# Optimization experiments

Hardware: AMD Instinct MI355X
Metric: run time of the kernel (lower is better)

The kernel has to match this reference:

```python
import jax, jax.numpy as jnp
import numpy as np
import math

HEAD_DIM = 128
NUM_Q_HEAD = 32
NUM_KV_HEAD = 8
WINDOW = 512
CAP = 30.0
CLIP_LO, CLIP_HI = -0.03, 1.03
EPS = 1e-5
SCALE = 1.0 / math.sqrt(HEAD_DIM)
B, S = 2, 2048


def group_rms_norm(x, w, group_size, eps):
    # x: [B, S, hidden]; normalize each contiguous group of size group_size
    Bx, Sx, H = x.shape
    ng = H // group_size
    xg = x.reshape(Bx, Sx, ng, group_size)
    inv = jax.lax.rsqrt(jnp.mean(xg * xg, axis=-1, keepdims=True) + eps)
    return (xg * inv).reshape(Bx, Sx, H) * w


def setup_inputs() -> dict:
    key = jax.random.key(0)
    kq, kk, kv, kw1, kw2 = jax.random.split(key, 5)
    q = jax.random.normal(kq, (B, S, NUM_Q_HEAD, HEAD_DIM), dtype=jnp.float32)
    k = jax.random.normal(kk, (B, S, NUM_KV_HEAD, HEAD_DIM), dtype=jnp.float32)
    v = jax.random.normal(kv, (B, S, NUM_KV_HEAD, HEAD_DIM), dtype=jnp.float32)
    # GroupRMSNorm weights, init uniform in (-1, 1)
    q_norm_w = jax.random.uniform(kw1, (NUM_Q_HEAD * HEAD_DIM,), dtype=jnp.float32, minval=-1.0, maxval=1.0)
    kv_norm_w = jax.random.uniform(kw2, (NUM_KV_HEAD * HEAD_DIM,), dtype=jnp.float32, minval=-1.0, maxval=1.0)
    return {"q": q, "k": k, "v": v, "q_norm_w": q_norm_w, "kv_norm_w": kv_norm_w}


def reference(q, k, v, q_norm_w, kv_norm_w):
    Bq, Sq, Hq, D = q.shape
    Sk = k.shape[1]
    # QK GroupRMSNorm over flattened hidden dim, group_size = head_dim
    qn = group_rms_norm(q.reshape(Bq, Sq, Hq * D), q_norm_w, HEAD_DIM, EPS).reshape(q.shape)
    kn = group_rms_norm(k.reshape(Bq, Sk, NUM_KV_HEAD * D), kv_norm_w, HEAD_DIM, EPS).reshape(k.shape)
    # GQA: repeat_interleave kv heads along head axis
    rep = Hq // NUM_KV_HEAD
    kr = jnp.repeat(kn, rep, axis=2)  # [B, Sk, Hq, D]
    vr = jnp.repeat(v, rep, axis=2)
    # scores: [B, Hq, Sq, Sk]
    scores = jnp.einsum("bqhd,bkhd->bhqk", qn, kr) * SCALE
    scores = CAP * jnp.tanh(scores / CAP)  # softmax capping
    # sliding-window + causal mask: allowed iff i - WINDOW <= j <= i (offset = Sk - Sq = 0)
    offset = Sk - Sq
    i = jnp.arange(Sq)[:, None] + offset
    j = jnp.arange(Sk)[None, :]
    allowed = (j <= i) & (j >= i - WINDOW)
    scores = jnp.where(allowed, scores, -jnp.inf)
    probs = jax.nn.softmax(scores, axis=-1)
    probs = jnp.nan_to_num(probs, nan=0.0)
    # softmax clipping
    probs = jnp.clip((CLIP_HI - CLIP_LO) * probs + CLIP_LO, 0.0, 1.0)
    out = jnp.einsum("bhqk,bkhd->bqhd", probs, vr)
    return out
```

## Files before the change

### kernel.cpp

```cpp
#include <hip/hip_runtime.h>

#define SEQ 2048
#define DD 128
#define HQ 32
#define HKV 8
#define WIN 512

typedef unsigned short u16;
typedef unsigned int u32;
typedef unsigned long long u64;
typedef __attribute__((ext_vector_type(8))) short bf16x8;
typedef __attribute__((ext_vector_type(4))) float f32x4;
typedef __attribute__((ext_vector_type(2))) float f32x2;

#define SBAR() asm volatile("s_barrier" ::: "memory")
#define WAITV0() asm volatile("s_waitcnt vmcnt(0)" ::: "memory")
#define WAITV4() asm volatile("s_waitcnt vmcnt(4)" ::: "memory")
#define WAITLGKM0() asm volatile("s_waitcnt lgkmcnt(0)" ::: "memory")

__device__ __forceinline__ u16 f2bf(float f) {
  u32 u = __builtin_bit_cast(u32, f);
  u += 0x7FFFu + ((u >> 16) & 1u);
  return (u16)(u >> 16);
}

__device__ __forceinline__ void gl16(const void* g, void* l) {
  __builtin_amdgcn_global_load_lds(
      (const __attribute__((address_space(1))) void*)g,
      (__attribute__((address_space(3))) void*)l, 16, 0, 0);
}

__device__ __forceinline__ u32 cvtpk(float lo, float hi) {
  u32 r;
  asm("v_cvt_pk_bf16_f32 %0, %1, %2" : "=v"(r) : "v"(lo), "v"(hi));
  return r;
}

__device__ __forceinline__ f32x2 pk_mul(f32x2 a, f32x2 b) {
  f32x2 d;
  asm("v_pk_mul_f32 %0, %1, %2" : "=v"(d) : "v"(a), "v"(b));
  return d;
}
__device__ __forceinline__ f32x2 pk_fma(f32x2 a, f32x2 b, f32x2 c) {
  f32x2 d;
  asm("v_pk_fma_f32 %0, %1, %2, %3" : "=v"(d) : "v"(a), "v"(b), "v"(c));
  return d;
}
__device__ __forceinline__ f32x2 pk_add(f32x2 a, f32x2 b) {
  f32x2 d;
  asm("v_pk_add_f32 %0, %1, %2" : "=v"(d) : "v"(a), "v"(b));
  return d;
}

__device__ __forceinline__ f32x2 score2(f32x2 x, f32x2 vL2E, f32x2 vmCE, f32x2 vmCTL) {
  f32x2 x2 = pk_mul(x, x);
  f32x2 a1 = pk_fma(x, vL2E, vmCE);
  f32x2 b1 = pk_mul(x2, vmCTL);
  return pk_fma(b1, x, a1);
}

__device__ __forceinline__ f32x2 unpk(u32 wv) {
  f32x2 r;
  r[0] = __builtin_bit_cast(float, wv << 16);
  r[1] = __builtin_bit_cast(float, wv & 0xFFFF0000u);
  return r;
}

__device__ __forceinline__ void norm_body(
    const float* __restrict__ x, const float* __restrict__ w,
    u16* __restrict__ o, int hshift, int blk, int tid) {
  const int lane = tid & 63;
  const int wv = tid >> 6;
  const int sub = lane >> 5;
  const int l5 = lane & 31;
  const int rid = blk * 8 + wv * 2 + sub;
  const int H = 1 << hshift;
  const int hh = rid & (H - 1);
  const int s = (rid >> hshift) & (SEQ - 1);
  const int b = rid >> (hshift + 11);
  const float4 xv = *(reinterpret_cast<const float4*>(x + (size_t)rid * DD) + l5);
  float ssq = xv.x * xv.x + xv.y * xv.y + xv.z * xv.z + xv.w * xv.w;
  ssq += __shfl_xor(ssq, 1);
  ssq += __shfl_xor(ssq, 2);
  ssq += __shfl_xor(ssq, 4);
  ssq += __shfl_xor(ssq, 8);
  ssq += __shfl_xor(ssq, 16);
  const float inv = rsqrtf(ssq * (1.0f / 128.0f) + 1e-5f);
  const float4 wv4 = *(reinterpret_cast<const float4*>(w + hh * DD) + l5);
  const u16 o0 = f2bf(xv.x * inv * wv4.x);
  const u16 o1 = f2bf(xv.y * inv * wv4.y);
  const u16 o2 = f2bf(xv.z * inv * wv4.z);
  const u16 o3 = f2bf(xv.w * inv * wv4.w);
  const size_t oo = (((size_t)b * H + hh) * SEQ + s) * DD + l5 * 4;
  uint2 pk;
  pk.x = (u32)o0 | ((u32)o1 << 16);
  pk.y = (u32)o2 | ((u32)o3 << 16);
  *reinterpret_cast<uint2*>(o + oo) = pk;
}

__device__ __forceinline__ void transv_body(
    const float* __restrict__ v, u16* __restrict__ vt, int bid, int t) {
  const int st = bid & 31;
  const int h = (bid >> 5) & 7;
  const int b = bid >> 8;
  const int sbase = st * 64;
  const int d = t & 127;
  const int sch = (t >> 7) * 32;
  const size_t oo = (((size_t)(b * HKV + h)) * DD + d) * SEQ + sbase + sch;
#pragma unroll
  for (int q8 = 0; q8 < 4; ++q8) {
    uint4 o;
    u32 c[4];
#pragma unroll
    for (int p = 0; p < 4; ++p) {
      const int ss0 = q8 * 8 + p * 2;
      const int s0 = sbase + sch + ss0;
      const float a0 = v[((size_t)(b * SEQ + s0) * HKV + h) * DD + d];
      const float a1 = v[((size_t)(b * SEQ + s0 + 1) * HKV + h) * DD + d];
      c[p] = (u32)f2bf(a0) | ((u32)f2bf(a1) << 16);
    }
    o.x = c[0]; o.y = c[1]; o.z = c[2]; o.w = c[3];
    *reinterpret_cast<uint4*>(vt + oo + q8 * 8) = o;
  }
}

__global__ void __launch_bounds__(256) prep_kernel(
    const float* __restrict__ k, const float* __restrict__ v,
    const float* __restrict__ kw, u16* __restrict__ kn, u16* __restrict__ vt) {
  const int blk = blockIdx.x;
  const int tid = threadIdx.x;
  if (blk < 4096) {
    norm_body(k, kw, kn, 3, blk, tid);
  } else {
    transv_body(v, vt, blk - 4096, tid);
  }
}

__global__ void __launch_bounds__(256, 3) attn_kernel(
    const float* __restrict__ q32, const float* __restrict__ qw,
    const u16* __restrict__ kn, const u16* __restrict__ vt,
    float* __restrict__ out) {
  __shared__ char smem[49168];
  const int tid = threadIdx.x;
  const int w = tid >> 6;
  const int lane = tid & 63;
  const int c = lane & 15;
  const int g = lane >> 4;

  const int p = blockIdx.x;
  const int bid = ((p & 7) << 8) + (p >> 3);
  const int qt = (bid & 127) ^ 127;
  const int hk = (bid >> 7) & 7;
  const int b = bid >> 10;
  const int i0 = qt * 16;
  const int h = hk * 4 + w;

  const u16* kbp = kn + (size_t)(b * HKV + hk) * SEQ * DD;
  const u16* vbp = vt + (size_t)(b * HKV + hk) * DD * SEQ;

  int ks = i0 - WIN;
  ks = (ks < 0) ? 0 : (ks & ~63);
  const int ntl = (i0 + 16 - ks + 63) >> 6;

  auto stageK = [&](int kb, int bufoff) {
    char* dst = smem + bufoff;
#pragma unroll
    for (int ci = 0; ci < 4; ++ci) {
      const int call = w * 4 + ci;
      const int row = call * 4 + g;
      const int ch = c ^ (row & 7);
      gl16(kbp + (size_t)(kb + row) * DD + ch * 8, dst + call * 1024);
    }
  };
  auto stageV = [&](int kb, int bufoff) {
    char* dst = smem + bufoff;
#pragma unroll
    for (int ci = 0; ci < 4; ++ci) {
      const int call = w * 4 + ci;
      const int vrow = call * 8 + (lane >> 3);
      const int vch = (lane & 7) ^ (vrow & 7);
      gl16(vbp + (size_t)vrow * SEQ + kb + vch * 8, dst + call * 1024);
    }
  };

  const float* qf = q32 + (((size_t)b * SEQ + i0 + c) * HQ + h) * DD;
  const float* wf = qw + h * DD;
  f32x4 qx[4][2];
#pragma unroll
  for (int kt = 0; kt < 4; ++kt) {
    qx[kt][0] = __builtin_nontemporal_load(
        reinterpret_cast<const f32x4*>(qf + kt * 32 + g * 8));
    qx[kt][1] = __builtin_nontemporal_load(
        reinterpret_cast<const f32x4*>(qf + kt * 32 + g * 8 + 4));
  }
  f32x4 qwv[4][2];
#pragma unroll
  for (int kt = 0; kt < 4; ++kt) {
    qwv[kt][0] = *reinterpret_cast<const f32x4*>(wf + kt * 32 + g * 8);
    qwv[kt][1] = *reinterpret_cast<const f32x4*>(wf + kt * 32 + g * 8 + 4);
  }

  stageK(ks, 0);
  if (ntl > 1) stageK(ks + 64, 16384);

  union AQ { bf16x8 v; u32 w4[4]; };
  AQ aq[4];
  {
    float ss = 0.0f;
#pragma unroll
    for (int kt = 0; kt < 4; ++kt) {
#pragma unroll
      for (int half = 0; half < 2; ++half) {
        const f32x4 a = qx[kt][half];
        ss = fmaf(a[0], a[0], ss); ss = fmaf(a[1], a[1], ss);
        ss = fmaf(a[2], a[2], ss); ss = fmaf(a[3], a[3], ss);
      }
    }
    ss += __shfl_xor(ss, 16);
    ss += __shfl_xor(ss, 32);
    const float inv = rsqrtf(ss * (1.0f / 128.0f) + 1e-5f) * 0.08838834764831845f;
#pragma unroll
    for (int kt = 0; kt < 4; ++kt) {
      const f32x4 a0 = qx[kt][0];
      const f32x4 a1 = qx[kt][1];
      const f32x4 w0 = qwv[kt][0];
      const f32x4 w1 = qwv[kt][1];
      aq[kt].w4[0] = cvtpk(a0[0] * inv * w0[0], a0[1] * inv * w0[1]);
      aq[kt].w4[1] = cvtpk(a0[2] * inv * w0[2], a0[3] * inv * w0[3]);
      aq[kt].w4[2] = cvtpk(a1[0] * inv * w1[0], a1[1] * inv * w1[1]);
      aq[kt].w4[3] = cvtpk(a1[2] * inv * w1[2], a1[3] * inv * w1[3]);
    }
  }

  const f32x2 vL2E = {1.44269504088896f, 1.44269504088896f};
  const f32x2 vmCE = {-43.2808512266689f, -43.2808512266689f};
  const f32x2 vmCTL = {-5.343315e-4f, -5.343315e-4f};

  u32 ebuf[9][8];
  f32x2 lsum2 = {0.0f, 0.0f};

#pragma unroll
  for (int t = 0; t < 9; ++t) {
    if (t >= ntl) continue;
    const int kb = ks + t * 64;
    if (t + 1 < ntl) { WAITV4(); } else { WAITV0(); }
    SBAR();
    if (t + 2 < ntl) stageK(kb + 128, ((t + 2) % 3) << 14);

    const char* kbuf = smem + ((t % 3) << 14);
    f32x4 sc[4] = {};
    __builtin_amdgcn_s_setprio(1);
#pragma unroll
    for (int nt = 0; nt < 4; ++nt) {
      const int jb = kb + nt * 16;
      if (jb > i0 + 15 || jb + 15 < i0 - WIN) continue;
      const int row = nt * 16 + c;
      const int sw = row & 7;
      const char* base = kbuf + row * 256;
#pragma unroll
      for (int kt = 0; kt < 4; ++kt) {
        const bf16x8 bk = *reinterpret_cast<const bf16x8*>(base + (((kt * 4 + g) ^ sw) << 4));
        sc[nt] = __builtin_amdgcn_mfma_f32_16x16x32_bf16(bk, aq[kt].v, sc[nt], 0, 0, 0);
      }
    }
    __builtin_amdgcn_s_setprio(0);

#pragma unroll
    for (int nt = 0; nt < 4; ++nt) {
      const int jb = kb + nt * 16;
      if (jb > i0 + 15 || jb + 15 < i0 - WIN) {
        ebuf[t][nt * 2] = 0;
        ebuf[t][nt * 2 + 1] = 0;
        continue;
      }
      const bool needmask = (jb + 15 > i0) || (jb < i0 + 15 - WIN);
      f32x2 lo = __builtin_shufflevector(sc[nt], sc[nt], 0, 1);
      f32x2 hi = __builtin_shufflevector(sc[nt], sc[nt], 2, 3);
      const f32x2 a0 = score2(lo, vL2E, vmCE, vmCTL);
      const f32x2 a1 = score2(hi, vL2E, vmCE, vmCTL);
      float e0 = __builtin_amdgcn_exp2f(a0[0]);
      float e1 = __builtin_amdgcn_exp2f(a0[1]);
      float e2 = __builtin_amdgcn_exp2f(a1[0]);
      float e3 = __builtin_amdgcn_exp2f(a1[1]);
      if (needmask) {
        const int difg = i0 + c - jb - g * 4;
        e0 = ((u32)(difg - 0) <= WIN) ? e0 : 0.0f;
        e1 = ((u32)(difg - 1) <= WIN) ? e1 : 0.0f;
        e2 = ((u32)(difg - 2) <= WIN) ? e2 : 0.0f;
        e3 = ((u32)(difg - 3) <= WIN) ? e3 : 0.0f;
      }
      ebuf[t][nt * 2] = cvtpk(e0, e1);
      ebuf[t][nt * 2 + 1] = cvtpk(e2, e3);
      const f32x2 eA = {e0, e1};
      const f32x2 eB = {e2, e3};
      lsum2 = pk_add(lsum2, pk_add(eA, eB));
    }
  }

  float l = lsum2[0] + lsum2[1];
  l += __shfl_xor(l, 16);
  l += __shfl_xor(l, 32);
  const float ar = 1.06f / l;
  const float thr = 0.0283018868f * l;

  u32 m9w = 0;
#pragma unroll
  for (int t = 0; t < 9; ++t) {
    if (t >= ntl) continue;
    bool nz = false;
#pragma unroll
    for (int u = 0; u < 8; ++u) {
      const f32x2 ef = unpk(ebuf[t][u]);
      nz = nz || (ef[0] > thr) || (ef[1] > thr);
    }
    if (__any(nz)) m9w |= 1u << t;
  }

  u32* mk = reinterpret_cast<u32*>(smem + 49152);
  mk[w] = m9w;
  WAITLGKM0();
  SBAR();
  const u32 m9 = mk[0] | mk[1] | mk[2] | mk[3];

  u64 nxtp = 0xFULL << 36;
  {
    int nx = 15;
#pragma unroll
    for (int t = 8; t >= 0; --t) {
      if (m9 & (1u << t)) nx = t;
      nxtp |= (u64)nx << (4 * t);
    }
  }
  const int f0 = (int)(nxtp & 15);
  if (f0 < 9) stageV(ks + f0 * 64, 0);

  const f32x2 var2 = {ar, ar};
  const f32x2 vm003 = {-0.03f, -0.03f};

  f32x4 acc[8] = {};
  int vi = 0;

#pragma unroll
  for (int t = 0; t < 9; ++t) {
    if (t >= ntl) continue;
    if (!(m9 & (1u << t))) continue;
    const int kb = ks + t * 64;
    WAITV0();
    SBAR();
    const int nx2 = (int)((nxtp >> (4 * (t + 1))) & 15);
    if (nx2 < 9) stageV(ks + nx2 * 64, ((vi + 1) & 1) << 14);
    const char* ldsV = smem + ((vi & 1) << 14);

#pragma unroll
    for (int k2 = 0; k2 < 2; ++k2) {
      const int jb2 = kb + k2 * 32;
      if (jb2 > i0 + 15 || jb2 + 31 < i0 - WIN) continue;

      u32 cw[4];
#pragma unroll
      for (int u = 0; u < 4; ++u) {
        const f32x2 ef = unpk(ebuf[t][k2 * 4 + u]);
        const f32x2 pr = pk_fma(ef, var2, vm003);
        cw[u] = cvtpk(__builtin_amdgcn_fmed3f(pr[0], 0.0f, 1.0f),
                      __builtin_amdgcn_fmed3f(pr[1], 0.0f, 1.0f));
      }

      const u32 nz = (cw[0] | cw[1]) | (cw[2] | cw[3]);
      if (!__any(nz != 0)) continue;

      union PU { bf16x8 v; u32 w4[4]; };
      PU pf;
      {
        u32 x0 = cw[0], y0 = cw[2];
        asm("v_permlane32_swap_b32 %0, %1" : "+v"(x0), "+v"(y0));
        asm("v_permlane16_swap_b32 %0, %1" : "+v"(x0), "+v"(y0));
        u32 x1 = cw[1], y1 = cw[3];
        asm("v_permlane32_swap_b32 %0, %1" : "+v"(x1), "+v"(y1));
        asm("v_permlane16_swap_b32 %0, %1" : "+v"(x1), "+v"(y1));
        pf.w4[0] = x0;
        pf.w4[1] = x1;
        pf.w4[2] = y0;
        pf.w4[3] = y1;
      }

      __builtin_amdgcn_s_setprio(1);
#pragma unroll
      for (int dt = 0; dt < 8; ++dt) {
        const int rv = dt * 16 + c;
        const bf16x8 bv = *reinterpret_cast<const bf16x8*>(
            ldsV + rv * 128 + (((k2 * 4 + g) ^ (rv & 7)) << 4));
        acc[dt] = __builtin_amdgcn_mfma_f32_16x16x32_bf16(pf.v, bv, acc[dt], 0, 0, 0);
      }
      __builtin_amdgcn_s_setprio(0);
    }
    ++vi;
  }

#pragma unroll
  for (int r = 0; r < 4; ++r) {
    const int i = i0 + g * 4 + r;
    float* op = out + (((size_t)b * SEQ + i) * HQ + h) * DD + c;
#pragma unroll
    for (int dt = 0; dt < 8; ++dt)
      __builtin_nontemporal_store(acc[dt][r], op + dt * 16);
  }
}

extern "C" void kernel_launch(void* const* d_in, const int* in_sizes, int n_in,
                              void* d_out, int out_size, void* d_ws, size_t ws_size,
                              hipStream_t stream) {
  const float* q = (const float*)d_in[0];
  const float* k = (const float*)d_in[1];
  const float* v = (const float*)d_in[2];
  const float* qw = (const float*)d_in[3];
  const float* kw = (const float*)d_in[4];
  float* out = (float*)d_out;

  u16* kn = (u16*)d_ws;
  u16* vt = kn + (size_t)2 * HKV * SEQ * DD;

  prep_kernel<<<4608, 256, 0, stream>>>(k, v, kw, kn, vt);
  attn_kernel<<<2048, 256, 0, stream>>>(q, qw, kn, vt, out);
}
```

Measured before the change: 75.67 us.

## Split key tiles across wave pairs, each wave computing two heads

Each wave now handles two query heads over half of each 64-key tile instead of one head over the whole tile. Each loaded K/V fragment from LDS then feeds two MFMAs, which halves LDS reads per MFMA. Row sums are exchanged between paired waves through shared memory, and the partial outputs are reduced through LDS before the global store. This doubles the accumulator and register footprint, so the occupancy hint drops from 3 to 2 blocks per CU, and it adds extra barriers and an LDS reduction at the end.

```diff
diff --git a/kernel.cpp b/kernel.cpp
--- a/kernel.cpp
+++ b/kernel.cpp
@@ -44,11 +44,6 @@
 __device__ __forceinline__ f32x2 pk_fma(f32x2 a, f32x2 b, f32x2 c) {
   f32x2 d;
   asm("v_pk_fma_f32 %0, %1, %2, %3" : "=v"(d) : "v"(a), "v"(b), "v"(c));
-  return d;
-}
-__device__ __forceinline__ f32x2 pk_add(f32x2 a, f32x2 b) {
-  f32x2 d;
-  asm("v_pk_add_f32 %0, %1, %2" : "=v"(d) : "v"(a), "v"(b));
   return d;
 }
 
@@ -136,16 +131,18 @@
   }
 }
 
-__global__ void __launch_bounds__(256, 3) attn_kernel(
+__global__ void __launch_bounds__(256, 2) attn_kernel(
     const float* __restrict__ q32, const float* __restrict__ qw,
     const u16* __restrict__ kn, const u16* __restrict__ vt,
     float* __restrict__ out) {
-  __shared__ char smem[49168];
+  __shared__ char smem[49696];
   const int tid = threadIdx.x;
   const int w = tid >> 6;
   const int lane = tid & 63;
   const int c = lane & 15;
   const int g = lane >> 4;
+  const int pr = w >> 1;
+  const int kh = w & 1;
 
   const int p = blockIdx.x;
   const int bid = ((p & 7) << 8) + (p >> 3);
@@ -153,7 +150,7 @@
   const int hk = (bid >> 7) & 7;
   const int b = bid >> 10;
   const int i0 = qt * 16;
-  const int h = hk * 4 + w;
+  const int h0 = hk * 4 + pr * 2;
 
   const u16* kbp = kn + (size_t)(b * HKV + hk) * SEQ * DD;
   const u16* vbp = vt + (size_t)(b * HKV + hk) * DD * SEQ;
@@ -183,52 +180,48 @@
     }
   };
 
-  const float* qf = q32 + (((size_t)b * SEQ + i0 + c) * HQ + h) * DD;
-  const float* wf = qw + h * DD;
-  f32x4 qx[4][2];
-#pragma unroll
-  for (int kt = 0; kt < 4; ++kt) {
-    qx[kt][0] = __builtin_nontemporal_load(
-        reinterpret_cast<const f32x4*>(qf + kt * 32 + g * 8));
-    qx[kt][1] = __builtin_nontemporal_load(
-        reinterpret_cast<const f32x4*>(qf + kt * 32 + g * 8 + 4));
-  }
-  f32x4 qwv[4][2];
-#pragma unroll
-  for (int kt = 0; kt < 4; ++kt) {
-    qwv[kt][0] = *reinterpret_cast<const f32x4*>(wf + kt * 32 + g * 8);
-    qwv[kt][1] = *reinterpret_cast<const f32x4*>(wf + kt * 32 + g * 8 + 4);
-  }
+  const float* qf0 = q32 + (((size_t)b * SEQ + i0 + c) * HQ + h0) * DD;
+  f32x4 qx[2][4][2];
+#pragma unroll
+  for (int hd = 0; hd < 2; ++hd)
+#pragma unroll
+    for (int kt = 0; kt < 4; ++kt) {
+      qx[hd][kt][0] = __builtin_nontemporal_load(
+          reinterpret_cast<const f32x4*>(qf0 + hd * DD + kt * 32 + g * 8));
+      qx[hd][kt][1] = __builtin_nontemporal_load(
+          reinterpret_cast<const f32x4*>(qf0 + hd * DD + kt * 32 + g * 8 + 4));
+    }
 
   stageK(ks, 0);
   if (ntl > 1) stageK(ks + 64, 16384);
 
   union AQ { bf16x8 v; u32 w4[4]; };
-  AQ aq[4];
-  {
+  AQ aq[2][4];
+#pragma unroll
+  for (int hd = 0; hd < 2; ++hd) {
     float ss = 0.0f;
 #pragma unroll
-    for (int kt = 0; kt < 4; ++kt) {
-#pragma unroll
-      for (int half = 0; half < 2; ++half) {
-        const f32x4 a = qx[kt][half];
+    for (int kt = 0; kt < 4; ++kt)
+#pragma unroll
+      for (int hf = 0; hf < 2; ++hf) {
+        const f32x4 a = qx[hd][kt][hf];
         ss = fmaf(a[0], a[0], ss); ss = fmaf(a[1], a[1], ss);
         ss = fmaf(a[2], a[2], ss); ss = fmaf(a[3], a[3], ss);
       }
-    }
     ss += __shfl_xor(ss, 16);
     ss += __shfl_xor(ss, 32);
     const float inv = rsqrtf(ss * (1.0f / 128.0f) + 1e-5f) * 0.08838834764831845f;
+    const float* wfh = qw + (h0 + hd) * DD;
 #pragma unroll
     for (int kt = 0; kt < 4; ++kt) {
-      const f32x4 a0 = qx[kt][0];
-      const f32x4 a1 = qx[kt][1];
-      const f32x4 w0 = qwv[kt][0];
-      const f32x4 w1 = qwv[kt][1];
-      aq[kt].w4[0] = cvtpk(a0[0] * inv * w0[0], a0[1] * inv * w0[1]);
-      aq[kt].w4[1] = cvtpk(a0[2] * inv * w0[2], a0[3] * inv * w0[3]);
-      aq[kt].w4[2] = cvtpk(a1[0] * inv * w1[0], a1[1] * inv * w1[1]);
-      aq[kt].w4[3] = cvtpk(a1[2] * inv * w1[2], a1[3] * inv * w1[3]);
+      const f32x4 w0 = *reinterpret_cast<const f32x4*>(wfh + kt * 32 + g * 8);
+      const f32x4 w1 = *reinterpret_cast<const f32x4*>(wfh + kt * 32 + g * 8 + 4);
+      const f32x4 a0 = qx[hd][kt][0];
+      const f32x4 a1 = qx[hd][kt][1];
+      aq[hd][kt].w4[0] = cvtpk(a0[0] * inv * w0[0], a0[1] * inv * w0[1]);
+      aq[hd][kt].w4[1] = cvtpk(a0[2] * inv * w0[2], a0[3] * inv * w0[3]);
+      aq[hd][kt].w4[2] = cvtpk(a1[0] * inv * w1[0], a1[1] * inv * w1[1]);
+      aq[hd][kt].w4[3] = cvtpk(a1[2] * inv * w1[2], a1[3] * inv * w1[3]);
     }
   }
 
@@ -236,8 +229,30 @@
   const f32x2 vmCE = {-43.2808512266689f, -43.2808512266689f};
   const f32x2 vmCTL = {-5.343315e-4f, -5.343315e-4f};
 
-  u32 ebuf[9][8];
-  f32x2 lsum2 = {0.0f, 0.0f};
+  u32 ebuf[9][2][4];
+  float lsum[2] = {0.0f, 0.0f};
+
+  auto doNT = [&](const f32x4& scv, int jb, u32& o0, u32& o1, float& ls) {
+    const bool needmask = (jb + 15 > i0) || (jb < i0 + 15 - WIN);
+    f32x2 lo = __builtin_shufflevector(scv, scv, 0, 1);
+    f32x2 hi = __builtin_shufflevector(scv, scv, 2, 3);
+    const f32x2 a0 = score2(lo, vL2E, vmCE, vmCTL);
+    const f32x2 a1 = score2(hi, vL2E, vmCE, vmCTL);
+    float e0 = __builtin_amdgcn_exp2f(a0[0]);
+    float e1 = __builtin_amdgcn_exp2f(a0[1]);
+    float e2 = __builtin_amdgcn_exp2f(a1[0]);
+    float e3 = __builtin_amdgcn_exp2f(a1[1]);
+    if (needmask) {
+      const int difg = i0 + c - jb - g * 4;
+      e0 = ((u32)(difg - 0) <= WIN) ? e0 : 0.0f;
+      e1 = ((u32)(difg - 1) <= WIN) ? e1 : 0.0f;
+      e2 = ((u32)(difg - 2) <= WIN) ? e2 : 0.0f;
+      e3 = ((u32)(difg - 3) <= WIN) ? e3 : 0.0f;
+    }
+    o0 = cvtpk(e0, e1);
+    o1 = cvtpk(e2, e3);
+    ls += (e0 + e1) + (e2 + e3);
+  };
 
 #pragma unroll
   for (int t = 0; t < 9; ++t) {
@@ -248,10 +263,11 @@
     if (t + 2 < ntl) stageK(kb + 128, ((t + 2) % 3) << 14);
 
     const char* kbuf = smem + ((t % 3) << 14);
-    f32x4 sc[4] = {};
+    f32x4 sc[2][2] = {};
     __builtin_amdgcn_s_setprio(1);
 #pragma unroll
-    for (int nt = 0; nt < 4; ++nt) {
+    for (int n = 0; n < 2; ++n) {
+      const int nt = kh * 2 + n;
       const int jb = kb + nt * 16;
       if (jb > i0 + 15 || jb + 15 < i0 - WIN) continue;
       const int row = nt * 16 + c;
@@ -260,48 +276,46 @@
 #pragma unroll
       for (int kt = 0; kt < 4; ++kt) {
         const bf16x8 bk = *reinterpret_cast<const bf16x8*>(base + (((kt * 4 + g) ^ sw) << 4));
-        sc[nt] = __builtin_amdgcn_mfma_f32_16x16x32_bf16(bk, aq[kt].v, sc[nt], 0, 0, 0);
+        sc[0][n] = __builtin_amdgcn_mfma_f32_16x16x32_bf16(bk, aq[0][kt].v, sc[0][n], 0, 0, 0);
+        sc[1][n] = __builtin_amdgcn_mfma_f32_16x16x32_bf16(bk, aq[1][kt].v, sc[1][n], 0, 0, 0);
       }
     }
     __builtin_amdgcn_s_setprio(0);
 
 #pragma unroll
-    for (int nt = 0; nt < 4; ++nt) {
-      const int jb = kb + nt * 16;
-      if (jb > i0 + 15 || jb + 15 < i0 - WIN) {
-        ebuf[t][nt * 2] = 0;
-        ebuf[t][nt * 2 + 1] = 0;
-        continue;
-      }
-      const bool needmask = (jb + 15 > i0) || (jb < i0 + 15 - WIN);
-      f32x2 lo = __builtin_shufflevector(sc[nt], sc[nt], 0, 1);
-      f32x2 hi = __builtin_shufflevector(sc[nt], sc[nt], 2, 3);
-      const f32x2 a0 = score2(lo, vL2E, vmCE, vmCTL);
-      const f32x2 a1 = score2(hi, vL2E, vmCE, vmCTL);
-      float e0 = __builtin_amdgcn_exp2f(a0[0]);
-      float e1 = __builtin_amdgcn_exp2f(a0[1]);
-      float e2 = __builtin_amdgcn_exp2f(a1[0]);
-      float e3 = __builtin_amdgcn_exp2f(a1[1]);
-      if (needmask) {
-        const int difg = i0 + c - jb - g * 4;
-        e0 = ((u32)(difg - 0) <= WIN) ? e0 : 0.0f;
-        e1 = ((u32)(difg - 1) <= WIN) ? e1 : 0.0f;
-        e2 = ((u32)(difg - 2) <= WIN) ? e2 : 0.0f;
-        e3 = ((u32)(difg - 3) <= WIN) ? e3 : 0.0f;
-      }
-      ebuf[t][nt * 2] = cvtpk(e0, e1);
-      ebuf[t][nt * 2 + 1] = cvtpk(e2, e3);
-      const f32x2 eA = {e0, e1};
-      const f32x2 eB = {e2, e3};
-      lsum2 = pk_add(lsum2, pk_add(eA, eB));
-    }
-  }
-
-  float l = lsum2[0] + lsum2[1];
-  l += __shfl_xor(l, 16);
-  l += __shfl_xor(l, 32);
-  const float ar = 1.06f / l;
-  const float thr = 0.0283018868f * l;
+    for (int hd = 0; hd < 2; ++hd)
+#pragma unroll
+      for (int n = 0; n < 2; ++n) {
+        const int nt = kh * 2 + n;
+        const int jb = kb + nt * 16;
+        if (jb > i0 + 15 || jb + 15 < i0 - WIN) {
+          ebuf[t][hd][n * 2] = 0;
+          ebuf[t][hd][n * 2 + 1] = 0;
+          continue;
+        }
+        doNT(sc[hd][n], jb, ebuf[t][hd][n * 2], ebuf[t][hd][n * 2 + 1], lsum[hd]);
+      }
+  }
+
+  float lw[2];
+#pragma unroll
+  for (int hd = 0; hd < 2; ++hd) {
+    float l = lsum[hd];
+    l += __shfl_xor(l, 16);
+    l += __shfl_xor(l, 32);
+    lw[hd] = l;
+  }
+  float* ls = reinterpret_cast<float*>(smem + 49152);
+  if (g == 0) {
+    ls[w * 32 + c] = lw[0];
+    ls[w * 32 + 16 + c] = lw[1];
+  }
+  WAITLGKM0();
+  SBAR();
+  const float l0 = lw[0] + ls[(w ^ 1) * 32 + c];
+  const float l1 = lw[1] + ls[(w ^ 1) * 32 + 16 + c];
+  const float ar0 = 1.06f / l0, thr0 = 0.0283018868f * l0;
+  const float ar1 = 1.06f / l1, thr1 = 0.0283018868f * l1;
 
   u32 m9w = 0;
 #pragma unroll
@@ -309,14 +323,14 @@
     if (t >= ntl) continue;
     bool nz = false;
 #pragma unroll
-    for (int u = 0; u < 8; ++u) {
-      const f32x2 ef = unpk(ebuf[t][u]);
-      nz = nz || (ef[0] > thr) || (ef[1] > thr);
+    for (int u = 0; u < 4; ++u) {
+      const f32x2 e0 = unpk(ebuf[t][0][u]);
+      const f32x2 e1 = unpk(ebuf[t][1][u]);
+      nz = nz || (e0[0] > thr0) || (e0[1] > thr0) || (e1[0] > thr1) || (e1[1] > thr1);
     }
     if (__any(nz)) m9w |= 1u << t;
   }
-
-  u32* mk = reinterpret_cast<u32*>(smem + 49152);
+  u32* mk = reinterpret_cast<u32*>(smem + 49664);
   mk[w] = m9w;
   WAITLGKM0();
   SBAR();
@@ -334,11 +348,23 @@
   const int f0 = (int)(nxtp & 15);
   if (f0 < 9) stageV(ks + f0 * 64, 0);
 
-  const f32x2 var2 = {ar, ar};
+  const f32x2 var0 = {ar0, ar0}, var1 = {ar1, ar1};
   const f32x2 vm003 = {-0.03f, -0.03f};
 
-  f32x4 acc[8] = {};
+  f32x4 acc[2][8] = {};
   int vi = 0;
+  const int hg = kh * 4 + g;
+
+  union PU { bf16x8 v; u32 w4[4]; };
+  auto mkPF = [&](const u32 cw[4], PU& pf) {
+    u32 x0 = cw[0], y0 = cw[2];
+    asm("v_permlane32_swap_b32 %0, %1" : "+v"(x0), "+v"(y0));
+    asm("v_permlane16_swap_b32 %0, %1" : "+v"(x0), "+v"(y0));
+    u32 x1 = cw[1], y1 = cw[3];
+    asm("v_permlane32_swap_b32 %0, %1" : "+v"(x1), "+v"(y1));
+    asm("v_permlane16_swap_b32 %0, %1" : "+v"(x1), "+v"(y1));
+    pf.w4[0] = x0; pf.w4[1] = x1; pf.w4[2] = y0; pf.w4[3] = y1;
+  };
 
 #pragma unroll
   for (int t = 0; t < 9; ++t) {
@@ -350,60 +376,93 @@
     const int nx2 = (int)((nxtp >> (4 * (t + 1))) & 15);
     if (nx2 < 9) stageV(ks + nx2 * 64, ((vi + 1) & 1) << 14);
     const char* ldsV = smem + ((vi & 1) << 14);
-
-#pragma unroll
-    for (int k2 = 0; k2 < 2; ++k2) {
-      const int jb2 = kb + k2 * 32;
-      if (jb2 > i0 + 15 || jb2 + 31 < i0 - WIN) continue;
-
-      u32 cw[4];
-#pragma unroll
-      for (int u = 0; u < 4; ++u) {
-        const f32x2 ef = unpk(ebuf[t][k2 * 4 + u]);
-        const f32x2 pr = pk_fma(ef, var2, vm003);
-        cw[u] = cvtpk(__builtin_amdgcn_fmed3f(pr[0], 0.0f, 1.0f),
-                      __builtin_amdgcn_fmed3f(pr[1], 0.0f, 1.0f));
-      }
-
-      const u32 nz = (cw[0] | cw[1]) | (cw[2] | cw[3]);
-      if (!__any(nz != 0)) continue;
-
-      union PU { bf16x8 v; u32 w4[4]; };
-      PU pf;
-      {
-        u32 x0 = cw[0], y0 = cw[2];
-        asm("v_permlane32_swap_b32 %0, %1" : "+v"(x0), "+v"(y0));
-        asm("v_permlane16_swap_b32 %0, %1" : "+v"(x0), "+v"(y0));
-        u32 x1 = cw[1], y1 = cw[3];
-        asm("v_permlane32_swap_b32 %0, %1" : "+v"(x1), "+v"(y1));
-        asm("v_permlane16_swap_b32 %0, %1" : "+v"(x1), "+v"(y1));
-        pf.w4[0] = x0;
-        pf.w4[1] = x1;
-        pf.w4[2] = y0;
-        pf.w4[3] = y1;
-      }
-
-      __builtin_amdgcn_s_setprio(1);
+    ++vi;
+
+    const int jb2 = kb + kh * 32;
+    if (jb2 > i0 + 15 || jb2 + 31 < i0 - WIN) continue;
+
+    u32 cw0[4], cw1[4];
+#pragma unroll
+    for (int u = 0; u < 4; ++u) {
+      const f32x2 e0 = unpk(ebuf[t][0][u]);
+      const f32x2 p0 = pk_fma(e0, var0, vm003);
+      cw0[u] = cvtpk(__builtin_amdgcn_fmed3f(p0[0], 0.0f, 1.0f),
+                     __builtin_amdgcn_fmed3f(p0[1], 0.0f, 1.0f));
+      const f32x2 e1 = unpk(ebuf[t][1][u]);
+      const f32x2 p1 = pk_fma(e1, var1, vm003);
+      cw1[u] = cvtpk(__builtin_amdgcn_fmed3f(p1[0], 0.0f, 1.0f),
+                     __builtin_amdgcn_fmed3f(p1[1], 0.0f, 1.0f));
+    }
+    const bool a0 = __any(((cw0[0] | cw0[1]) | (cw0[2] | cw0[3])) != 0);
+    const bool a1 = __any(((cw1[0] | cw1[1]) | (cw1[2] | cw1[3])) != 0);
+    if (!a0 && !a1) continue;
+
+    PU pf0, pf1;
+    if (a0) mkPF(cw0, pf0);
+    if (a1) mkPF(cw1, pf1);
+
+    __builtin_amdgcn_s_setprio(1);
+    if (a0 && a1) {
 #pragma unroll
       for (int dt = 0; dt < 8; ++dt) {
         const int rv = dt * 16 + c;
         const bf16x8 bv = *reinterpret_cast<const bf16x8*>(
-            ldsV + rv * 128 + (((k2 * 4 + g) ^ (rv & 7)) << 4));
-        acc[dt] = __builtin_amdgcn_mfma_f32_16x16x32_bf16(pf.v, bv, acc[dt], 0, 0, 0);
-      }
-      __builtin_amdgcn_s_setprio(0);
-    }
-    ++vi;
-  }
-
-#pragma unroll
-  for (int r = 0; r < 4; ++r) {
-    const int i = i0 + g * 4 + r;
-    float* op = out + (((size_t)b * SEQ + i) * HQ + h) * DD + c;
+            ldsV + rv * 128 + ((hg ^ (rv & 7)) << 4));
+        acc[0][dt] = __builtin_amdgcn_mfma_f32_16x16x32_bf16(pf0.v, bv, acc[0][dt], 0, 0, 0);
+        acc[1][dt] = __builtin_amdgcn_mfma_f32_16x16x32_bf16(pf1.v, bv, acc[1][dt], 0, 0, 0);
+      }
+    } else if (a0) {
+#pragma unroll
+      for (int dt = 0; dt < 8; ++dt) {
+        const int rv = dt * 16 + c;
+        const bf16x8 bv = *reinterpret_cast<const bf16x8*>(
+            ldsV + rv * 128 + ((hg ^ (rv & 7)) << 4));
+        acc[0][dt] = __builtin_amdgcn_mfma_f32_16x16x32_bf16(pf0.v, bv, acc[0][dt], 0, 0, 0);
+      }
+    } else {
+#pragma unroll
+      for (int dt = 0; dt < 8; ++dt) {
+        const int rv = dt * 16 + c;
+        const bf16x8 bv = *reinterpret_cast<const bf16x8*>(
+            ldsV + rv * 128 + ((hg ^ (rv & 7)) << 4));
+        acc[1][dt] = __builtin_amdgcn_mfma_f32_16x16x32_bf16(pf1.v, bv, acc[1][dt], 0, 0, 0);
+      }
+    }
+    __builtin_amdgcn_s_setprio(0);
+  }
+
+  auto dumpAcc = [&](const f32x4 (&a)[8], char* slot) {
 #pragma unroll
     for (int dt = 0; dt < 8; ++dt)
-      __builtin_nontemporal_store(acc[dt][r], op + dt * 16);
-  }
+#pragma unroll
+      for (int r = 0; r < 4; ++r) {
+        const int word = (4 * g + r) * 128 + ((dt ^ (g & 1)) << 4) + c;
+        *reinterpret_cast<float*>(slot + word * 4) = a[dt][r];
+      }
+  };
+  auto finishAcc = [&](const f32x4 (&a)[8], const char* slot, int h) {
+#pragma unroll
+    for (int r = 0; r < 4; ++r) {
+      const int i = i0 + 4 * g + r;
+      float* op = out + (((size_t)b * SEQ + i) * HQ + h) * DD + c;
+#pragma unroll
+      for (int dt = 0; dt < 8; ++dt) {
+        const int word = (4 * g + r) * 128 + ((dt ^ (g & 1)) << 4) + c;
+        const float v = a[dt][r] + *reinterpret_cast<const float*>(slot + word * 4);
+        __builtin_nontemporal_store(v, op + dt * 16);
+      }
+    }
+  };
+
+  SBAR();
+  char* slotW = smem + pr * 16384 + (kh ^ 1) * 8192;
+  if (kh == 0) dumpAcc(acc[1], slotW);
+  else         dumpAcc(acc[0], slotW);
+  WAITLGKM0();
+  SBAR();
+  const char* slotR = smem + pr * 16384 + kh * 8192;
+  if (kh == 0) finishAcc(acc[0], slotR, h0);
+  else         finishAcc(acc[1], slotR, h0 + 1);
 }
 
 extern "C" void kernel_launch(void* const* d_in, const int* in_sizes, int n_in,
```

Result: slower. 96.62 us (+27.7%).

## Stage V in compacted 32-key half tiles, batched six per barrier

Applied to the files above, without the earlier changes.

The skip mask for V tiles moves from 64-key granularity to 32-key halves, so only halves with non-negligible probabilities are loaded. Live halves are compacted into up to six 8 KB LDS slots and issued together, then one wait and barrier precede the MFMA pass. This replaces the per-tile double-buffered wait/barrier chain with fewer synchronisation points and cuts wasted V loads. In exchange all loads in a chunk are exposed before any compute starts, so load latency is no longer overlapped with MFMAs. The LDS layout and read swizzle for V also change.

```diff
diff --git a/kernel.cpp b/kernel.cpp
--- a/kernel.cpp
+++ b/kernel.cpp
@@ -172,14 +172,16 @@
       gl16(kbp + (size_t)(kb + row) * DD + ch * 8, dst + call * 1024);
     }
   };
-  auto stageV = [&](int kb, int bufoff) {
-    char* dst = smem + bufoff;
-#pragma unroll
-    for (int ci = 0; ci < 4; ++ci) {
-      const int call = w * 4 + ci;
-      const int vrow = call * 8 + (lane >> 3);
-      const int vch = (lane & 7) ^ (vrow & 7);
-      gl16(vbp + (size_t)vrow * SEQ + kb + vch * 8, dst + call * 1024);
+  auto stageVhalf = [&](int kb32, int slot) {
+    char* dst = smem + slot * 8192;
+#pragma unroll
+    for (int ci = 0; ci < 2; ++ci) {
+      const int call = w * 2 + ci;
+      const int row = call * 8 + (lane >> 3);
+      const int col = (lane & 7) ^ (row & 7);
+      const int d = row * 2 + (col >> 2);
+      const int kc = col & 3;
+      gl16(vbp + (size_t)d * SEQ + kb32 + kc * 8, dst + call * 1024);
     }
   };
 
@@ -303,97 +305,101 @@
   const float ar = 1.06f / l;
   const float thr = 0.0283018868f * l;
 
-  u32 m9w = 0;
+  u32 m18w = 0;
 #pragma unroll
   for (int t = 0; t < 9; ++t) {
     if (t >= ntl) continue;
-    bool nz = false;
-#pragma unroll
-    for (int u = 0; u < 8; ++u) {
-      const f32x2 ef = unpk(ebuf[t][u]);
-      nz = nz || (ef[0] > thr) || (ef[1] > thr);
-    }
-    if (__any(nz)) m9w |= 1u << t;
-  }
-
-  u32* mk = reinterpret_cast<u32*>(smem + 49152);
-  mk[w] = m9w;
-  WAITLGKM0();
-  SBAR();
-  const u32 m9 = mk[0] | mk[1] | mk[2] | mk[3];
-
-  u64 nxtp = 0xFULL << 36;
-  {
-    int nx = 15;
-#pragma unroll
-    for (int t = 8; t >= 0; --t) {
-      if (m9 & (1u << t)) nx = t;
-      nxtp |= (u64)nx << (4 * t);
-    }
-  }
-  const int f0 = (int)(nxtp & 15);
-  if (f0 < 9) stageV(ks + f0 * 64, 0);
-
-  const f32x2 var2 = {ar, ar};
-  const f32x2 vm003 = {-0.03f, -0.03f};
-
-  f32x4 acc[8] = {};
-  int vi = 0;
-
-#pragma unroll
-  for (int t = 0; t < 9; ++t) {
-    if (t >= ntl) continue;
-    if (!(m9 & (1u << t))) continue;
     const int kb = ks + t * 64;
-    WAITV0();
-    SBAR();
-    const int nx2 = (int)((nxtp >> (4 * (t + 1))) & 15);
-    if (nx2 < 9) stageV(ks + nx2 * 64, ((vi + 1) & 1) << 14);
-    const char* ldsV = smem + ((vi & 1) << 14);
-
 #pragma unroll
     for (int k2 = 0; k2 < 2; ++k2) {
       const int jb2 = kb + k2 * 32;
       if (jb2 > i0 + 15 || jb2 + 31 < i0 - WIN) continue;
-
-      u32 cw[4];
+      bool nz = false;
 #pragma unroll
       for (int u = 0; u < 4; ++u) {
         const f32x2 ef = unpk(ebuf[t][k2 * 4 + u]);
-        const f32x2 pr = pk_fma(ef, var2, vm003);
-        cw[u] = cvtpk(__builtin_amdgcn_fmed3f(pr[0], 0.0f, 1.0f),
-                      __builtin_amdgcn_fmed3f(pr[1], 0.0f, 1.0f));
-      }
-
-      const u32 nz = (cw[0] | cw[1]) | (cw[2] | cw[3]);
-      if (!__any(nz != 0)) continue;
-
-      union PU { bf16x8 v; u32 w4[4]; };
-      PU pf;
-      {
-        u32 x0 = cw[0], y0 = cw[2];
-        asm("v_permlane32_swap_b32 %0, %1" : "+v"(x0), "+v"(y0));
-        asm("v_permlane16_swap_b32 %0, %1" : "+v"(x0), "+v"(y0));
-        u32 x1 = cw[1], y1 = cw[3];
-        asm("v_permlane32_swap_b32 %0, %1" : "+v"(x1), "+v"(y1));
-        asm("v_permlane16_swap_b32 %0, %1" : "+v"(x1), "+v"(y1));
-        pf.w4[0] = x0;
-        pf.w4[1] = x1;
-        pf.w4[2] = y0;
-        pf.w4[3] = y1;
-      }
-
-      __builtin_amdgcn_s_setprio(1);
-#pragma unroll
-      for (int dt = 0; dt < 8; ++dt) {
-        const int rv = dt * 16 + c;
-        const bf16x8 bv = *reinterpret_cast<const bf16x8*>(
-            ldsV + rv * 128 + (((k2 * 4 + g) ^ (rv & 7)) << 4));
-        acc[dt] = __builtin_amdgcn_mfma_f32_16x16x32_bf16(pf.v, bv, acc[dt], 0, 0, 0);
-      }
-      __builtin_amdgcn_s_setprio(0);
-    }
-    ++vi;
+        nz = nz || (ef[0] > thr) || (ef[1] > thr);
+      }
+      if (__any(nz)) m18w |= 1u << (t * 2 + k2);
+    }
+  }
+
+  u32* mk = reinterpret_cast<u32*>(smem + 49152);
+  mk[w] = m18w;
+  WAITLGKM0();
+  SBAR();
+  const u32 m18 = mk[0] | mk[1] | mk[2] | mk[3];
+  const int nh = __builtin_popcount(m18);
+
+  const f32x2 var2 = {ar, ar};
+  const f32x2 vm003 = {-0.03f, -0.03f};
+
+  f32x4 acc[8] = {};
+
+  union PU { bf16x8 v; u32 w4[4]; };
+  for (int ch = 0; ch < 3; ++ch) {
+    const int base = ch * 6;
+    if (base >= nh) break;
+
+#pragma unroll
+    for (int t = 0; t < 9; ++t) {
+#pragma unroll
+      for (int k2 = 0; k2 < 2; ++k2) {
+        const int ht = t * 2 + k2;
+        if (!((m18 >> ht) & 1)) continue;
+        const int st = __builtin_popcount(m18 & ((1u << ht) - 1u));
+        if (st < base || st >= base + 6) continue;
+        stageVhalf(ks + t * 64 + k2 * 32, st - base);
+      }
+    }
+    WAITV0();
+    SBAR();
+
+#pragma unroll
+    for (int t = 0; t < 9; ++t) {
+#pragma unroll
+      for (int k2 = 0; k2 < 2; ++k2) {
+        const int ht = t * 2 + k2;
+        if (!((m18 >> ht) & 1)) continue;
+        const int st = __builtin_popcount(m18 & ((1u << ht) - 1u));
+        if (st < base || st >= base + 6) continue;
+        const char* ldsV = smem + (st - base) * 8192;
+
+        u32 cw[4];
+#pragma unroll
+        for (int u = 0; u < 4; ++u) {
+          const f32x2 ef = unpk(ebuf[t][k2 * 4 + u]);
+          const f32x2 pr = pk_fma(ef, var2, vm003);
+          cw[u] = cvtpk(__builtin_amdgcn_fmed3f(pr[0], 0.0f, 1.0f),
+                        __builtin_amdgcn_fmed3f(pr[1], 0.0f, 1.0f));
+        }
+        const u32 nzv = (cw[0] | cw[1]) | (cw[2] | cw[3]);
+        if (!__any(nzv != 0)) continue;
+
+        PU pf;
+        {
+          u32 x0 = cw[0], y0 = cw[2];
+          asm("v_permlane32_swap_b32 %0, %1" : "+v"(x0), "+v"(y0));
+          asm("v_permlane16_swap_b32 %0, %1" : "+v"(x0), "+v"(y0));
+          u32 x1 = cw[1], y1 = cw[3];
+          asm("v_permlane32_swap_b32 %0, %1" : "+v"(x1), "+v"(y1));
+          asm("v_permlane16_swap_b32 %0, %1" : "+v"(x1), "+v"(y1));
+          pf.w4[0] = x0; pf.w4[1] = x1; pf.w4[2] = y0; pf.w4[3] = y1;
+        }
+
+        __builtin_amdgcn_s_setprio(1);
+#pragma unroll
+        for (int dt = 0; dt < 8; ++dt) {
+          const int rowv = dt * 8 + (c >> 1);
+          const int colv = (c & 1) * 4 + g;
+          const bf16x8 bv = *reinterpret_cast<const bf16x8*>(
+              ldsV + rowv * 128 + ((colv ^ (rowv & 7)) << 4));
+          acc[dt] = __builtin_amdgcn_mfma_f32_16x16x32_bf16(pf.v, bv, acc[dt], 0, 0, 0);
+        }
+        __builtin_amdgcn_s_setprio(0);
+      }
+    }
+    if (base + 6 < nh) SBAR();
   }
 
 #pragma unroll
```

Result: slower. 103.9 us (+37.3%).
